# Kernel optimization log

Hardware: AMD Instinct MI355X
Metric: run time of the kernel (lower is better)

The kernel has to match this reference:

```python
import jax, jax.numpy as jnp
import numpy as np

H = 3584        # hidden_size
NH = 16         # num_attention_heads
HD = 256        # head_dim
NKV = 8         # num_key_value_heads
GROUPS = NH // NKV
B, S = 2, 2048
SOFTCAP = 50.0
SCALE = 256.0 ** -0.5   # query_pre_attn_scalar ** -0.5
ROPE_BASE = 10000.0
NEG = -1e9


def _rotate_half(x):
    x1, x2 = jnp.split(x, 2, axis=-1)
    return jnp.concatenate([-x2, x1], axis=-1)


def _apply_rope(x, cos, sin):
    # x: [b, h, s, d]; cos/sin: [s, d]
    return x * cos[None, None] + _rotate_half(x) * sin[None, None]


def setup_inputs() -> dict:
    key = jax.random.key(0)
    k1, k2, k3, k4, k5 = jax.random.split(key, 5)
    hidden_states = jax.random.normal(k1, (B, S, H), dtype=jnp.float32)
    # additive causal mask [1, 1, S, S]
    causal = jnp.tril(jnp.ones((S, S), dtype=bool))
    attention_mask = jnp.where(causal, 0.0, NEG).astype(jnp.float32)[None, None]
    Wq = jax.random.normal(k2, (H, NH * HD), dtype=jnp.float32) * 0.02
    Wk = jax.random.normal(k3, (H, NKV * HD), dtype=jnp.float32) * 0.02
    Wv = jax.random.normal(k4, (H, NKV * HD), dtype=jnp.float32) * 0.02
    Wo = jax.random.normal(k5, (NH * HD, H), dtype=jnp.float32) * 0.02
    return {"hidden_states": hidden_states, "attention_mask": attention_mask,
            "Wq": Wq, "Wk": Wk, "Wv": Wv, "Wo": Wo}


def reference(hidden_states, attention_mask, Wq, Wk, Wv, Wo):
    b, s, _ = hidden_states.shape
    q = (hidden_states @ Wq).reshape(b, s, NH, HD).transpose(0, 2, 1, 3)   # [b,nh,s,d]
    k = (hidden_states @ Wk).reshape(b, s, NKV, HD).transpose(0, 2, 1, 3)  # [b,nkv,s,d]
    v = (hidden_states @ Wv).reshape(b, s, NKV, HD).transpose(0, 2, 1, 3)

    # RoPE (HF-style: freqs duplicated, rotate_half)
    pos = jnp.arange(s, dtype=jnp.float32)
    inv_freq = 1.0 / (ROPE_BASE ** (jnp.arange(0, HD, 2, dtype=jnp.float32) / HD))
    freqs = pos[:, None] * inv_freq[None, :]          # [s, d/2]
    emb = jnp.concatenate([freqs, freqs], axis=-1)    # [s, d]
    cos, sin = jnp.cos(emb), jnp.sin(emb)
    q = _apply_rope(q, cos, sin)
    k = _apply_rope(k, cos, sin)

    # repeat_kv for GQA
    k = jnp.repeat(k, GROUPS, axis=1)  # [b,nh,s,d]
    v = jnp.repeat(v, GROUPS, axis=1)

    scores = jnp.einsum('bhsd,bhtd->bhst', q, k) * SCALE
    # tanh logit softcapping
    scores = jnp.tanh(scores / SOFTCAP) * SOFTCAP
    scores = scores + attention_mask
    probs = jax.nn.softmax(scores.astype(jnp.float32), axis=-1).astype(q.dtype)
    out = jnp.einsum('bhst,bhtd->bhsd', probs, v)
    out = out.transpose(0, 2, 1, 3).reshape(b, s, NH * HD)
    return out @ Wo
```

## Files before the change

kernel.cpp:

```cpp
#include <hip/hip_runtime.h>
#include <cstdint>
#include <cstddef>

typedef __bf16 bf16x8 __attribute__((ext_vector_type(8)));
typedef float  f32x4  __attribute__((ext_vector_type(4)));
typedef unsigned short u16;

#define GLDS16(GP, LP) __builtin_amdgcn_global_load_lds( \
    (const __attribute__((address_space(1))) void*)(GP), \
    (__attribute__((address_space(3))) void*)(LP), 16, 0, 0)

__device__ __forceinline__ float b2f(u16 u) {
  unsigned int x = ((unsigned int)u) << 16;
  return __builtin_bit_cast(float, x);
}
__device__ __forceinline__ u16 f2b(float f) {
  unsigned int u = __builtin_bit_cast(unsigned int, f);
  unsigned int r = (u + 0x7fffu + ((u >> 16) & 1u)) >> 16;
  return (u16)r;
}

constexpr int Bc  = 2;
constexpr int Sc  = 2048;
constexpr int Hc  = 3584;
constexpr int NHc = 16;
constexpr int HDc = 256;
constexpr int NKV = 8;
constexpr int QD  = NHc * HDc;
constexpr int QS  = 8192;
constexpr float SCALE   = 0.0625f;
constexpr float CAP     = 50.0f;
constexpr float INV_CAP = 1.0f / 50.0f;

__device__ __forceinline__ float softcap(float raw) {
  float y = raw * (SCALE * INV_CAP);
  float a = __builtin_fabsf(y);
  float e = __expf(-2.0f * a);
  float t = (1.0f - e) * __builtin_amdgcn_rcpf(1.0f + e);
  return copysignf(t, y) * CAP;
}

__global__ void rope_table_k(float* __restrict__ cosT, float* __restrict__ sinT) {
  int idx = blockIdx.x * 256 + threadIdx.x;
  int s = idx >> 7, i = idx & 127;
  float inv = expf((float)i * -0.0719557841560639f);
  float ang = (float)s * inv;
  cosT[idx] = cosf(ang);
  sinT[idx] = sinf(ang);
}

__global__ void cvt_f32_bf16(const float4* __restrict__ in, ushort4* __restrict__ out, int n4) {
  int i = blockIdx.x * 256 + threadIdx.x;
  int st = gridDim.x * 256;
  for (; i < n4; i += st) {
    float4 v = in[i];
    ushort4 u;
    u.x = f2b(v.x); u.y = f2b(v.y); u.z = f2b(v.z); u.w = f2b(v.w);
    out[i] = u;
  }
}

__global__ void transpose_cvt(const float* __restrict__ in, u16* __restrict__ out, int R, int C) {
  __shared__ float t[32][33];
  int c0 = blockIdx.x * 32, r0 = blockIdx.y * 32;
  int tx = threadIdx.x, ty = threadIdx.y;
#pragma unroll
  for (int i = 0; i < 4; i++)
    t[ty + i * 8][tx] = in[(size_t)(r0 + ty + i * 8) * C + c0 + tx];
  __syncthreads();
#pragma unroll
  for (int i = 0; i < 4; i++)
    out[(size_t)(c0 + ty + i * 8) * R + r0 + tx] = f2b(t[tx][ty + i * 8]);
}

__global__ void transpose_v(const u16* __restrict__ QKV, u16* __restrict__ Vt) {
  __shared__ u16 t[32][33];
  int b = blockIdx.z >> 3, kvh = blockIdx.z & 7;
  int s0 = blockIdx.x * 32, d0 = blockIdx.y * 32;
  int tx = threadIdx.x, ty = threadIdx.y;
#pragma unroll
  for (int i = 0; i < 4; i++)
    t[ty + i * 8][tx] = QKV[(size_t)(b * Sc + s0 + ty + i * 8) * QS + 6144 + kvh * HDc + d0 + tx];
  __syncthreads();
#pragma unroll
  for (int i = 0; i < 4; i++)
    Vt[(size_t)((b * NKV + kvh) * HDc + d0 + ty + i * 8) * Sc + s0 + tx] = t[tx][ty + i * 8];
}

template <int NH>
__global__ void rope_apply(u16* __restrict__ X, const float* __restrict__ cosT,
                           const float* __restrict__ sinT) {
  constexpr int LS = (NH == 16) ? 4 : 3;
  int idx = blockIdx.x * 256 + threadIdx.x;
  const int i4 = (idx & 31) << 2;
  const int h = (idx >> 5) & (NH - 1);
  const int row = idx >> (5 + LS);
  const int s = row & (Sc - 1);
  u16* p = X + (size_t)row * QS + h * 256 + i4;
  ushort4 lo = *(const ushort4*)p;
  ushort4 hi = *(const ushort4*)(p + 128);
  float4 c = *(const float4*)(cosT + s * 128 + i4);
  float4 sn = *(const float4*)(sinT + s * 128 + i4);
  ushort4 nlo, nhi;
  { float xl = b2f(lo.x), xh = b2f(hi.x);
    nlo.x = f2b(xl * c.x - xh * sn.x); nhi.x = f2b(xh * c.x + xl * sn.x); }
  { float xl = b2f(lo.y), xh = b2f(hi.y);
    nlo.y = f2b(xl * c.y - xh * sn.y); nhi.y = f2b(xh * c.y + xl * sn.y); }
  { float xl = b2f(lo.z), xh = b2f(hi.z);
    nlo.z = f2b(xl * c.z - xh * sn.z); nhi.z = f2b(xh * c.z + xl * sn.z); }
  { float xl = b2f(lo.w), xh = b2f(hi.w);
    nlo.w = f2b(xl * c.w - xh * sn.w); nhi.w = f2b(xh * c.w + xl * sn.w); }
  *(ushort4*)p = nlo;
  *(ushort4*)(p + 128) = nhi;
}

template <typename OT>
__global__ __launch_bounds__(512, 1) void gemm256(const u16* __restrict__ A,
                                                  const u16* __restrict__ Bt,
                                                  OT* __restrict__ C,
                                                  int M, int N, int K, int GM) {
  __shared__ alignas(16) u16 As[2][256 * 64];
  __shared__ alignas(16) u16 Bs[2][256 * 64];
  const int nwg = gridDim.x;
  const int cpx = nwg >> 3;
  const int wgid = (blockIdx.x & 7) * cpx + (blockIdx.x >> 3);
  const int GN = nwg / GM;
  const int width = 8 * GN;
  const int grp = wgid / width;
  const int rem = wgid - grp * width;
  const int m0 = (grp * 8 + (rem & 7)) * 256;
  const int n0 = (rem >> 3) * 256;
  const int tid = threadIdx.x;
  const int lane = tid & 63;
  const int w = tid >> 6;
  const int wm = w >> 2, wn = w & 3;
  const int lg = lane >> 4, lr = lane & 15;
  const int nkt = K >> 6;

  auto STAGE = [&](int buf, int kt) {
    const int k0 = kt * 64;
#pragma unroll
    for (int i = 0; i < 4; i++) {
      int c = i * 512 + tid;
      int row = c >> 3, slot = c & 7;
      GLDS16(A + (size_t)(m0 + row) * K + k0 + (slot ^ (row & 7)) * 8,
             (char*)As[buf] + c * 16);
    }
#pragma unroll
    for (int i = 0; i < 4; i++) {
      int c = i * 512 + tid;
      int row = c >> 3, slot = c & 7;
      GLDS16(Bt + (size_t)(n0 + row) * K + k0 + (slot ^ (row & 7)) * 8,
             (char*)Bs[buf] + c * 16);
    }
  };

  f32x4 acc[8][4] = {};

  STAGE(0, 0);
  STAGE(1, 1);
  asm volatile("s_waitcnt vmcnt(8)" ::: "memory");
  __builtin_amdgcn_sched_barrier(0);
  __builtin_amdgcn_s_barrier();

  for (int kt = 0; kt < nkt; ++kt) {
    const int buf = kt & 1;
    bf16x8 bfr[4][2], af[4][2];
#pragma unroll
    for (int j = 0; j < 4; j++)
#pragma unroll
      for (int ks = 0; ks < 2; ks++) {
        int row = wn * 64 + j * 16 + lr;
        int sl = (ks * 4 + lg) ^ (row & 7);
        bfr[j][ks] = *(const bf16x8*)&Bs[buf][row * 64 + sl * 8];
      }
#pragma unroll
    for (int i = 0; i < 4; i++)
#pragma unroll
      for (int ks = 0; ks < 2; ks++) {
        int row = wm * 128 + i * 16 + lr;
        int sl = (ks * 4 + lg) ^ (row & 7);
        af[i][ks] = *(const bf16x8*)&As[buf][row * 64 + sl * 8];
      }
    asm volatile("s_waitcnt lgkmcnt(0)" ::: "memory");
    __builtin_amdgcn_sched_barrier(0);
    __builtin_amdgcn_s_setprio(1);
#pragma unroll
    for (int i = 0; i < 4; i++)
#pragma unroll
      for (int j = 0; j < 4; j++)
#pragma unroll
        for (int ks = 0; ks < 2; ks++)
          acc[i][j] = __builtin_amdgcn_mfma_f32_16x16x32_bf16(
              af[i][ks], bfr[j][ks], acc[i][j], 0, 0, 0);
    __builtin_amdgcn_s_setprio(0);
#pragma unroll
    for (int i = 0; i < 4; i++)
#pragma unroll
      for (int ks = 0; ks < 2; ks++) {
        int row = wm * 128 + 64 + i * 16 + lr;
        int sl = (ks * 4 + lg) ^ (row & 7);
        af[i][ks] = *(const bf16x8*)&As[buf][row * 64 + sl * 8];
      }
    asm volatile("s_waitcnt lgkmcnt(0)" ::: "memory");
    __builtin_amdgcn_sched_barrier(0);
    __builtin_amdgcn_s_barrier();
    if (kt + 2 < nkt) STAGE(buf, kt + 2);
    __builtin_amdgcn_s_setprio(1);
#pragma unroll
    for (int i = 0; i < 4; i++)
#pragma unroll
      for (int j = 0; j < 4; j++)
#pragma unroll
        for (int ks = 0; ks < 2; ks++)
          acc[4 + i][j] = __builtin_amdgcn_mfma_f32_16x16x32_bf16(
              af[i][ks], bfr[j][ks], acc[4 + i][j], 0, 0, 0);
    __builtin_amdgcn_s_setprio(0);
    if (kt + 1 < nkt) {
      if (kt + 2 < nkt)
        asm volatile("s_waitcnt vmcnt(8)" ::: "memory");
      else
        asm volatile("s_waitcnt vmcnt(0)" ::: "memory");
      __builtin_amdgcn_sched_barrier(0);
      __builtin_amdgcn_s_barrier();
    }
  }

#pragma unroll
  for (int i = 0; i < 8; i++) {
    const int row = m0 + wm * 128 + i * 16 + lg * 4;
#pragma unroll
    for (int j = 0; j < 4; j++) {
      const int col = n0 + wn * 64 + j * 16 + lr;
#pragma unroll
      for (int r = 0; r < 4; r++) {
        if constexpr (sizeof(OT) == 2)
          C[(size_t)(row + r) * N + col] = f2b(acc[i][j][r]);
        else
          C[(size_t)(row + r) * N + col] = acc[i][j][r];
      }
    }
  }
}

__global__ __launch_bounds__(512, 1) void attn_fwd(const u16* __restrict__ QKV,
                                                   const u16* __restrict__ Vt,
                                                   u16* __restrict__ AO) {
  constexpr int KVB = 64;
  __shared__ alignas(16) u16 Ks[2][KVB * 256];
  __shared__ alignas(16) u16 Vs[2][256 * KVB];
  __shared__ alignas(16) u16 Ps[8][16][72];
  const int bx = blockIdx.x, h = blockIdx.y, b = blockIdx.z;
  const int qt = b ? (15 - bx) : bx;
  const int q0 = qt * 128;
  const int kvh = h >> 1;
  const int tid = threadIdx.x, w = tid >> 6, lane = tid & 63;
  const int lg = lane >> 4, lr = lane & 15;

  bf16x8 qf[8];
  {
    const u16* qp = QKV + (size_t)(b * Sc + q0 + w * 16 + lr) * QS + h * HDc + lg * 8;
#pragma unroll
    for (int kk = 0; kk < 8; kk++) qf[kk] = *(const bf16x8*)(qp + kk * 32);
  }

  f32x4 o[16] = {};
  float m_r[4], l_r[4];
#pragma unroll
  for (int r = 0; r < 4; r++) { m_r[r] = -1e30f; l_r[r] = 0.0f; }
  const int my_qrow = q0 + w * 16 + lg * 4;
  const int wave_min_row = q0 + w * 16;
  const int wave_max_row = q0 + w * 16 + 15;

  const u16* kbase = QKV + (size_t)(b * Sc) * QS + 4096 + kvh * HDc;
  const u16* vbase = Vt + (size_t)((b * NKV + kvh) * HDc) * Sc;

  auto STAGE = [&](int buf, int t0) {
#pragma unroll
    for (int i = 0; i < 4; i++) {
      int c = i * 512 + tid;
      int row = c >> 5, slot = c & 31;
      int gs = slot ^ (row & 7);
      GLDS16(kbase + (size_t)(t0 + row) * QS + gs * 8, (char*)Ks[buf] + c * 16);
    }
#pragma unroll
    for (int i = 0; i < 4; i++) {
      int c = i * 512 + tid;
      int d = c >> 3, slot = c & 7;
      int gs = slot ^ (d & 7);
      GLDS16(vbase + (size_t)d * Sc + t0 + gs * 8, (char*)Vs[buf] + c * 16);
    }
  };

  const int nt = 2 * qt + 2;
  int cur = 0;
  STAGE(0, 0);
  for (int ti = 0; ti < nt; ++ti) {
    const int t0 = ti * 64;
    if (ti + 1 < nt) {
      STAGE(cur ^ 1, t0 + 64);
      asm volatile("s_waitcnt vmcnt(8)" ::: "memory");
    } else {
      asm volatile("s_waitcnt vmcnt(0)" ::: "memory");
    }
    __builtin_amdgcn_sched_barrier(0);
    __builtin_amdgcn_s_barrier();

    if (t0 <= wave_max_row) {
      const u16* KsT = Ks[cur];
      const u16* VsT = Vs[cur];

      f32x4 sc[4];
#pragma unroll
      for (int j = 0; j < 4; j++) {
        f32x4 a = {0.f, 0.f, 0.f, 0.f};
        const int row = j * 16 + lr;
#pragma unroll
        for (int kk = 0; kk < 8; kk++) {
          int s0 = (kk * 4 + lg) ^ (lr & 7);
          bf16x8 kf = *(const bf16x8*)&KsT[row * 256 + s0 * 8];
          a = __builtin_amdgcn_mfma_f32_16x16x32_bf16(qf[kk], kf, a, 0, 0, 0);
        }
        sc[j] = a;
      }

      float tmax[4] = {-1e30f, -1e30f, -1e30f, -1e30f};
      if (t0 + 63 > wave_min_row) {
#pragma unroll
        for (int j = 0; j < 4; j++)
#pragma unroll
          for (int r = 0; r < 4; r++) {
            float x = softcap(sc[j][r]);
            if (t0 + j * 16 + lr > my_qrow + r) x = -1e9f;
            sc[j][r] = x;
            tmax[r] = fmaxf(tmax[r], x);
          }
      } else {
#pragma unroll
        for (int j = 0; j < 4; j++)
#pragma unroll
          for (int r = 0; r < 4; r++) {
            float x = softcap(sc[j][r]);
            sc[j][r] = x;
            tmax[r] = fmaxf(tmax[r], x);
          }
      }
#pragma unroll
      for (int xm = 1; xm < 16; xm <<= 1)
#pragma unroll
        for (int r = 0; r < 4; r++) tmax[r] = fmaxf(tmax[r], __shfl_xor(tmax[r], xm, 64));

      bool need = false;
#pragma unroll
      for (int r = 0; r < 4; r++) need |= (tmax[r] > m_r[r] + 8.0f);
      if (__any(need)) {
        float scal[4];
#pragma unroll
        for (int r = 0; r < 4; r++) {
          float mn = fmaxf(m_r[r], tmax[r]);
          scal[r] = __expf(m_r[r] - mn);
          m_r[r] = mn;
          l_r[r] *= scal[r];
        }
#pragma unroll
        for (int df = 0; df < 16; df++)
#pragma unroll
          for (int r = 0; r < 4; r++) o[df][r] *= scal[r];
      }

      float psum[4] = {0.f, 0.f, 0.f, 0.f};
#pragma unroll
      for (int j = 0; j < 4; j++)
#pragma unroll
        for (int r = 0; r < 4; r++) {
          float p = __expf(sc[j][r] - m_r[r]);
          psum[r] += p;
          Ps[w][lg * 4 + r][j * 16 + lr] = f2b(p);
        }
#pragma unroll
      for (int xm = 1; xm < 16; xm <<= 1)
#pragma unroll
        for (int r = 0; r < 4; r++) psum[r] += __shfl_xor(psum[r], xm, 64);
#pragma unroll
      for (int r = 0; r < 4; r++) l_r[r] += psum[r];

      bf16x8 pf0 = *(const bf16x8*)&Ps[w][lr][lg * 8];
      bf16x8 pf1 = *(const bf16x8*)&Ps[w][lr][32 + lg * 8];
#pragma unroll
      for (int df = 0; df < 16; df++) {
        const int d = df * 16 + lr;
        int s0 = lg ^ (lr & 7);
        int s1 = (4 + lg) ^ (lr & 7);
        bf16x8 vf0 = *(const bf16x8*)&VsT[d * KVB + s0 * 8];
        o[df] = __builtin_amdgcn_mfma_f32_16x16x32_bf16(pf0, vf0, o[df], 0, 0, 0);
        bf16x8 vf1 = *(const bf16x8*)&VsT[d * KVB + s1 * 8];
        o[df] = __builtin_amdgcn_mfma_f32_16x16x32_bf16(pf1, vf1, o[df], 0, 0, 0);
      }
    }

    __builtin_amdgcn_s_barrier();
    cur ^= 1;
  }

  float inv_l[4];
#pragma unroll
  for (int r = 0; r < 4; r++) inv_l[r] = 1.0f / l_r[r];
  u16* op = AO + (size_t)(b * Sc + my_qrow) * QD + h * HDc + lr;
#pragma unroll
  for (int df = 0; df < 16; df++)
#pragma unroll
    for (int r = 0; r < 4; r++)
      op[(size_t)r * QD + df * 16] = f2b(o[df][r] * inv_l[r]);
}

extern "C" void kernel_launch(void* const* d_in, const int* in_sizes, int n_in,
                              void* d_out, int out_size, void* d_ws, size_t ws_size,
                              hipStream_t stream) {
  (void)in_sizes; (void)n_in; (void)out_size; (void)ws_size;
  const float* hs = (const float*)d_in[0];
  const float* Wq = (const float*)d_in[2];
  const float* Wk = (const float*)d_in[3];
  const float* Wv = (const float*)d_in[4];
  const float* Wo = (const float*)d_in[5];
  float* out = (float*)d_out;
  char* ws = (char*)d_ws;

  float* cosT = (float*)(ws + 0);
  float* sinT = (float*)(ws + 1048576);
  u16* hsb    = (u16*)(ws + 2097152);
  u16* Wqkvt  = (u16*)(ws + 31457280);
  u16* Wot    = (u16*)(ws + 90177536);
  u16* QKVb   = (u16*)(ws + 119537664);
  u16* Vtr    = hsb;
  u16* AO     = Wqkvt;

  dim3 tb32x8(32, 8);

  rope_table_k<<<1024, 256, 0, stream>>>(cosT, sinT);
  cvt_f32_bf16<<<2048, 256, 0, stream>>>((const float4*)hs, (ushort4*)hsb, (Bc * Sc * Hc) / 4);
  transpose_cvt<<<dim3(QD / 32, Hc / 32), tb32x8, 0, stream>>>(Wq, Wqkvt, Hc, QD);
  transpose_cvt<<<dim3(2048 / 32, Hc / 32), tb32x8, 0, stream>>>(Wk, Wqkvt + (size_t)4096 * Hc, Hc, 2048);
  transpose_cvt<<<dim3(2048 / 32, Hc / 32), tb32x8, 0, stream>>>(Wv, Wqkvt + (size_t)6144 * Hc, Hc, 2048);
  transpose_cvt<<<dim3(Hc / 32, QD / 32), tb32x8, 0, stream>>>(Wo, Wot, QD, Hc);

  gemm256<u16><<<dim3(16 * 32), 512, 0, stream>>>(hsb, Wqkvt, QKVb, Bc * Sc, QS, Hc, 16);

  rope_apply<16><<<8192, 256, 0, stream>>>(QKVb, cosT, sinT);
  rope_apply<8><<<4096, 256, 0, stream>>>(QKVb + 4096, cosT, sinT);
  transpose_v<<<dim3(Sc / 32, HDc / 32, Bc * NKV), tb32x8, 0, stream>>>(QKVb, Vtr);

  attn_fwd<<<dim3(16, NHc, Bc), 512, 0, stream>>>(QKVb, Vtr, AO);

  gemm256<float><<<dim3(16 * 14), 512, 0, stream>>>(AO, Wot, out, Bc * Sc, Hc, QD, 16);
}
```

Before: 620.3 us.

## Split GEMM k-step into four quadrant phases with staggered A/B staging

Restructures the GEMM main loop into four MFMA phases (A-low/B-low, A-low/B-high, A-high/B-low, A-high/B-high), each preceded by its own LDS fragment loads and workgroup barriers. The B tile for step kt+2 is staged after B is fully read and the A tile after A is fully read, which spreads global-to-LDS traffic across the iteration in a ping-pong style. The goal is to interleave LDS reads, global loads and MFMA work more finely and shrink register pressure for B fragments. The cost is many more s_barriers per iteration, and buffer reuse has to stay correct with the split staging.

```diff
diff --git a/kernel.cpp b/kernel.cpp
--- a/kernel.cpp
+++ b/kernel.cpp
@@ -137,7 +137,7 @@
   const int lg = lane >> 4, lr = lane & 15;
   const int nkt = K >> 6;
 
-  auto STAGE = [&](int buf, int kt) {
+  auto STAGE_A = [&](int buf, int kt) {
     const int k0 = kt * 64;
 #pragma unroll
     for (int i = 0; i < 4; i++) {
@@ -146,6 +146,9 @@
       GLDS16(A + (size_t)(m0 + row) * K + k0 + (slot ^ (row & 7)) * 8,
              (char*)As[buf] + c * 16);
     }
+  };
+  auto STAGE_B = [&](int buf, int kt) {
+    const int k0 = kt * 64;
 #pragma unroll
     for (int i = 0; i < 4; i++) {
       int c = i * 512 + tid;
@@ -157,73 +160,104 @@
 
   f32x4 acc[8][4] = {};
 
-  STAGE(0, 0);
-  STAGE(1, 1);
+  STAGE_A(0, 0); STAGE_B(0, 0);
+  STAGE_A(1, 1); STAGE_B(1, 1);
   asm volatile("s_waitcnt vmcnt(8)" ::: "memory");
   __builtin_amdgcn_sched_barrier(0);
   __builtin_amdgcn_s_barrier();
 
   for (int kt = 0; kt < nkt; ++kt) {
     const int buf = kt & 1;
-    bf16x8 bfr[4][2], af[4][2];
-#pragma unroll
-    for (int j = 0; j < 4; j++)
+    const bool stg = (kt + 2 < nkt);
+    bf16x8 aL[4][2], aH[4][2], bL[2][2], bH[2][2];
+
+#pragma unroll
+    for (int i = 0; i < 4; i++)
+#pragma unroll
+      for (int ks = 0; ks < 2; ks++) {
+        int row = wm * 128 + i * 16 + lr;
+        aL[i][ks] = *(const bf16x8*)&As[buf][row * 64 + ((ks * 4 + lg) ^ (row & 7)) * 8];
+      }
+#pragma unroll
+    for (int j = 0; j < 2; j++)
 #pragma unroll
       for (int ks = 0; ks < 2; ks++) {
         int row = wn * 64 + j * 16 + lr;
-        int sl = (ks * 4 + lg) ^ (row & 7);
-        bfr[j][ks] = *(const bf16x8*)&Bs[buf][row * 64 + sl * 8];
-      }
-#pragma unroll
-    for (int i = 0; i < 4; i++)
-#pragma unroll
-      for (int ks = 0; ks < 2; ks++) {
-        int row = wm * 128 + i * 16 + lr;
-        int sl = (ks * 4 + lg) ^ (row & 7);
-        af[i][ks] = *(const bf16x8*)&As[buf][row * 64 + sl * 8];
-      }
+        bL[j][ks] = *(const bf16x8*)&Bs[buf][row * 64 + ((ks * 4 + lg) ^ (row & 7)) * 8];
+      }
+    __builtin_amdgcn_s_barrier();
     asm volatile("s_waitcnt lgkmcnt(0)" ::: "memory");
     __builtin_amdgcn_sched_barrier(0);
     __builtin_amdgcn_s_setprio(1);
 #pragma unroll
     for (int i = 0; i < 4; i++)
 #pragma unroll
-      for (int j = 0; j < 4; j++)
+      for (int j = 0; j < 2; j++)
 #pragma unroll
         for (int ks = 0; ks < 2; ks++)
-          acc[i][j] = __builtin_amdgcn_mfma_f32_16x16x32_bf16(
-              af[i][ks], bfr[j][ks], acc[i][j], 0, 0, 0);
+          acc[i][j] = __builtin_amdgcn_mfma_f32_16x16x32_bf16(aL[i][ks], bL[j][ks], acc[i][j], 0, 0, 0);
     __builtin_amdgcn_s_setprio(0);
+    __builtin_amdgcn_s_barrier();
+
+#pragma unroll
+    for (int j = 0; j < 2; j++)
+#pragma unroll
+      for (int ks = 0; ks < 2; ks++) {
+        int row = wn * 64 + 32 + j * 16 + lr;
+        bH[j][ks] = *(const bf16x8*)&Bs[buf][row * 64 + ((ks * 4 + lg) ^ (row & 7)) * 8];
+      }
+    __builtin_amdgcn_s_barrier();
+    asm volatile("s_waitcnt lgkmcnt(0)" ::: "memory");
+    __builtin_amdgcn_sched_barrier(0);
+    __builtin_amdgcn_s_setprio(1);
+#pragma unroll
+    for (int i = 0; i < 4; i++)
+#pragma unroll
+      for (int j = 0; j < 2; j++)
+#pragma unroll
+        for (int ks = 0; ks < 2; ks++)
+          acc[i][2 + j] = __builtin_amdgcn_mfma_f32_16x16x32_bf16(aL[i][ks], bH[j][ks], acc[i][2 + j], 0, 0, 0);
+    __builtin_amdgcn_s_setprio(0);
+    __builtin_amdgcn_s_barrier();
+
 #pragma unroll
     for (int i = 0; i < 4; i++)
 #pragma unroll
       for (int ks = 0; ks < 2; ks++) {
         int row = wm * 128 + 64 + i * 16 + lr;
-        int sl = (ks * 4 + lg) ^ (row & 7);
-        af[i][ks] = *(const bf16x8*)&As[buf][row * 64 + sl * 8];
-      }
+        aH[i][ks] = *(const bf16x8*)&As[buf][row * 64 + ((ks * 4 + lg) ^ (row & 7)) * 8];
+      }
+    if (stg) STAGE_B(buf, kt + 2);
+    __builtin_amdgcn_s_barrier();
     asm volatile("s_waitcnt lgkmcnt(0)" ::: "memory");
     __builtin_amdgcn_sched_barrier(0);
-    __builtin_amdgcn_s_barrier();
-    if (kt + 2 < nkt) STAGE(buf, kt + 2);
     __builtin_amdgcn_s_setprio(1);
 #pragma unroll
     for (int i = 0; i < 4; i++)
 #pragma unroll
-      for (int j = 0; j < 4; j++)
+      for (int j = 0; j < 2; j++)
 #pragma unroll
         for (int ks = 0; ks < 2; ks++)
-          acc[4 + i][j] = __builtin_amdgcn_mfma_f32_16x16x32_bf16(
-              af[i][ks], bfr[j][ks], acc[4 + i][j], 0, 0, 0);
+          acc[4 + i][j] = __builtin_amdgcn_mfma_f32_16x16x32_bf16(aH[i][ks], bL[j][ks], acc[4 + i][j], 0, 0, 0);
     __builtin_amdgcn_s_setprio(0);
-    if (kt + 1 < nkt) {
-      if (kt + 2 < nkt)
-        asm volatile("s_waitcnt vmcnt(8)" ::: "memory");
-      else
-        asm volatile("s_waitcnt vmcnt(0)" ::: "memory");
-      __builtin_amdgcn_sched_barrier(0);
-      __builtin_amdgcn_s_barrier();
-    }
+    __builtin_amdgcn_s_barrier();
+
+    if (stg) STAGE_A(buf, kt + 2);
+    __builtin_amdgcn_s_setprio(1);
+#pragma unroll
+    for (int i = 0; i < 4; i++)
+#pragma unroll
+      for (int j = 0; j < 2; j++)
+#pragma unroll
+        for (int ks = 0; ks < 2; ks++)
+          acc[4 + i][2 + j] = __builtin_amdgcn_mfma_f32_16x16x32_bf16(aH[i][ks], bH[j][ks], acc[4 + i][2 + j], 0, 0, 0);
+    __builtin_amdgcn_s_setprio(0);
+    if (stg)
+      asm volatile("s_waitcnt vmcnt(8)" ::: "memory");
+    else
+      asm volatile("s_waitcnt vmcnt(0)" ::: "memory");
+    __builtin_amdgcn_sched_barrier(0);
+    __builtin_amdgcn_s_barrier();
   }
 
 #pragma unroll
```

Result: slower. 637.1 us (+2.7%).
